# Performance work log

Measured on AMD Instinct MI355X. Metric: run time of the kernel, lower is better.

## Reference

```python
import jax, jax.numpy as jnp
import numpy as np

N, E, B = 100000, 400000, 2048     # nodes, edges, graphs
H, L = 300, 5                      # hidden_feats, n_layers
NT, EF, T = 120, 16, 128           # num_node_types, in_edge_feats, n_tasks
EPS = 1e-5                         # BatchNorm eps (eval mode, running_mean=0, running_var=1)


def setup_inputs() -> dict:
    key = jax.random.key(0)
    ks = jax.random.split(key, 16)
    g = lambda i, shape, s=0.05: jax.random.normal(ks[i], shape, jnp.float32) * s
    return dict(
        node_types=jax.random.randint(ks[0], (N,), 0, NT),
        src=jax.random.randint(ks[1], (E,), 0, N),
        dst=jax.random.randint(ks[2], (E,), 0, N),
        graph_ids=jnp.sort(jax.random.randint(ks[3], (N,), 0, B)),
        edge_feats=jax.random.normal(ks[4], (E, EF), jnp.float32),
        node_emb=g(5, (NT, H), 1.0),          # nn.Embedding(num_node_types, H)
        Wn=g(6, (L, H, H)), bn=g(7, (L, H), 0.01),      # per-layer node projection
        We=g(8, (L, EF, H)), be=g(9, (L, H), 0.01),     # per-layer edge projection
        root=g(10, (L, H)),                   # per-layer root embedding (Embedding(1,H))
        gamma=1.0 + g(11, (L, H), 0.01), beta=g(12, (L, H), 0.01),  # layer BN
        vn_emb=g(13, (H,)),                   # virtual node embedding (Embedding(1,H))
        W1=g(14, (L - 1, H, 2 * H)), b1=jnp.zeros((L - 1, 2 * H), jnp.float32),
        g1=jnp.ones((L - 1, 2 * H), jnp.float32), be1=jnp.zeros((L - 1, 2 * H), jnp.float32),
        W2=g(15, (L - 1, 2 * H, H)), b2=jnp.zeros((L - 1, H), jnp.float32),
        g2=jnp.ones((L - 1, H), jnp.float32), be2=jnp.zeros((L - 1, H), jnp.float32),
        pW=jax.random.normal(jax.random.fold_in(key, 99), (H, T), jnp.float32) * 0.05,
        pb=jnp.zeros((T,), jnp.float32),
    )


def _bn(x, ga, be_):
    # eval-mode BatchNorm1d with running_mean=0, running_var=1
    return x * (ga / jnp.sqrt(1.0 + EPS)) + be_


def reference(node_types, src, dst, graph_ids, edge_feats, node_emb,
              Wn, bn, We, be, root, gamma, beta, vn_emb,
              W1, b1, g1, be1, W2, b2, g2, be2, pW, pb):
    ones_e = jnp.ones((E,), jnp.float32)
    deg = jax.ops.segment_sum(ones_e, dst, num_segments=N) + 1.0   # in_degrees + 1
    norm = deg ** -0.5
    edge_norm = (norm[src] * norm[dst])[:, None]                   # (E, 1)
    inv_deg = (1.0 / deg)[:, None]                                 # (N, 1)

    h = node_emb[node_types]                      # (N, H) node encoder
    vn = jnp.broadcast_to(vn_emb, (B, H))         # (B, H) virtual node feats

    for l in range(L):
        h = h + vn[graph_ids]                     # dgl.broadcast_nodes
        x = h @ Wn[l] + bn[l]                     # (N, H)
        e = edge_feats @ We[l] + be[l]            # (E, H)
        m = edge_norm * jax.nn.relu(x[src] + e)   # per-edge messages
        agg = jax.ops.segment_sum(m, dst, num_segments=N)          # (N, H)
        out = agg + jax.nn.relu(x + root[l]) * inv_deg
        out = _bn(out, gamma[l], beta[l])
        if l != L - 1:
            out = jax.nn.relu(out)
        h_in = h                                  # h_list[l] (after vn broadcast add)
        h = out                                   # dropout p=0 -> identity; residual=False
        if l < L - 1:
            vtmp = jax.ops.segment_sum(h_in, graph_ids, num_segments=B) + vn
            z = jax.nn.relu(_bn(vtmp @ W1[l] + b1[l], g1[l], be1[l]))
            vn = jax.nn.relu(_bn(z @ W2[l] + b2[l], g2[l], be2[l]))

    # mean readout over each graph, then linear head
    counts = jax.ops.segment_sum(jnp.ones((N,), jnp.float32), graph_ids, num_segments=B)
    gsum = jax.ops.segment_sum(h, graph_ids, num_segments=B)
    gmean = gsum / jnp.maximum(counts, 1.0)[:, None]
    return gmean @ pW + pb                        # (B, n_tasks)
```

## Files before the change

kernel.cpp:

```cpp
#include <hip/hip_runtime.h>
#include <hip/hip_bf16.h>
#include <hip/hip_fp16.h>

#define N_ 100000
#define MPAD 100096
#define E_ 400000
#define B_ 2048
#define H_ 300
#define KP_ 320
#define L_ 5
#define EF_ 16
#define T_ 128
#define ANODES 8
#define EMAX 128
#define BNS 0.9999950000374997f

typedef unsigned short ushort_t;
typedef short bf16x8 __attribute__((ext_vector_type(8)));
typedef float f32x4 __attribute__((ext_vector_type(4)));
typedef _Float16 h2f __attribute__((ext_vector_type(2)));

__device__ __forceinline__ ushort_t f2b(float v) {
    unsigned u = __float_as_uint(v);
    unsigned r = (u + 0x7FFFu + ((u >> 16) & 1u)) >> 16;
    return (ushort_t)r;
}

__device__ __forceinline__ float b2f(ushort_t u) {
    return __uint_as_float(((unsigned)u) << 16);
}

__device__ __forceinline__ void gl_lds16(const void* g, void* l) {
    __builtin_amdgcn_global_load_lds(
        (const __attribute__((address_space(1))) void*)g,
        (__attribute__((address_space(3))) void*)l, 16, 0, 0);
}

__device__ __forceinline__ int swzcol(int r, int j) {
    int u = ((j >> 3) & 3) ^ ((r >> 1) & 3);
    return (j & ~31) | (u << 3) | (j & 7);
}

__global__ void k_hist(const int* __restrict__ dst, int* __restrict__ degi, int E) {
    int e = blockIdx.x * blockDim.x + threadIdx.x;
    if (e < E) atomicAdd(&degi[dst[e]], 1);
}

__global__ void k_norm(const int* __restrict__ degi, float* __restrict__ nrm,
                       float* __restrict__ invdeg, int N) {
    int n = blockIdx.x * blockDim.x + threadIdx.x;
    if (n < N) {
        float d = (float)degi[n] + 1.0f;
        nrm[n] = 1.0f / sqrtf(d);
        invdeg[n] = 1.0f / d;
    }
}

__global__ void k_scan1(const int* __restrict__ in, int* __restrict__ out,
                        int* __restrict__ partial, int N) {
    __shared__ int s[1024];
    int i = blockIdx.x * 1024 + threadIdx.x;
    int v = (i < N) ? in[i] : 0;
    s[threadIdx.x] = v;
    __syncthreads();
    for (int off = 1; off < 1024; off <<= 1) {
        int t = (threadIdx.x >= off) ? s[threadIdx.x - off] : 0;
        __syncthreads();
        s[threadIdx.x] += t;
        __syncthreads();
    }
    if (i < N) out[i] = s[threadIdx.x] - v;
    if (threadIdx.x == 1023) partial[blockIdx.x] = s[1023];
}

__global__ void k_scan2(int* __restrict__ partial, int nb, int* __restrict__ totalOut) {
    __shared__ int sh[128];
    int t = threadIdx.x;
    int v = (t < nb) ? partial[t] : 0;
    sh[t] = v;
    __syncthreads();
    for (int off = 1; off < 128; off <<= 1) {
        int u = (t >= off) ? sh[t - off] : 0;
        __syncthreads();
        sh[t] += u;
        __syncthreads();
    }
    if (t < nb) partial[t] = sh[t] - v;
    if (t == 127) *totalOut = sh[127];
}

__global__ void k_scan3(int* __restrict__ out, const int* __restrict__ partial, int N) {
    int i = blockIdx.x * 1024 + threadIdx.x;
    if (i < N) out[i] += partial[blockIdx.x];
}

__global__ void k_scatter(const int* __restrict__ dst, const int* __restrict__ src,
                          const float* __restrict__ ef, const float* __restrict__ nrm,
                          int* __restrict__ cursor, int2* __restrict__ meta,
                          ushort_t* __restrict__ ef16, int E) {
    int e = blockIdx.x * blockDim.x + threadIdx.x;
    if (e >= E) return;
    int d = dst[e], s = src[e];
    int pos = atomicAdd(&cursor[d], 1);
    int2 md;
    md.x = s * KP_;
    md.y = __float_as_int(nrm[s] * nrm[d]);
    meta[pos] = md;
    const float4* ep = (const float4*)&ef[(size_t)e * EF_];
    float4 e0 = ep[0], e1 = ep[1], e2 = ep[2], e3 = ep[3];
    uint4 ua, ub;
    ua.x = __builtin_bit_cast(unsigned, __floats2half2_rn(e0.x, e0.y));
    ua.y = __builtin_bit_cast(unsigned, __floats2half2_rn(e0.z, e0.w));
    ua.z = __builtin_bit_cast(unsigned, __floats2half2_rn(e1.x, e1.y));
    ua.w = __builtin_bit_cast(unsigned, __floats2half2_rn(e1.z, e1.w));
    ub.x = __builtin_bit_cast(unsigned, __floats2half2_rn(e2.x, e2.y));
    ub.y = __builtin_bit_cast(unsigned, __floats2half2_rn(e2.z, e2.w));
    ub.z = __builtin_bit_cast(unsigned, __floats2half2_rn(e3.x, e3.y));
    ub.w = __builtin_bit_cast(unsigned, __floats2half2_rn(e3.z, e3.w));
    uint4* op = (uint4*)&ef16[(size_t)pos * 16];
    op[0] = ua; op[1] = ub;
}

__global__ void k_rowstart(const int* __restrict__ gid, int* __restrict__ rs, int N, int B) {
    int b = blockIdx.x * blockDim.x + threadIdx.x;
    if (b <= B) {
        int lo = 0, hi = N;
        while (lo < hi) { int mid = (lo + hi) >> 1; if (gid[mid] < b) lo = mid + 1; else hi = mid; }
        rs[b] = lo;
    }
}

__global__ void k_hinit(const int* __restrict__ nt, const float* __restrict__ emb,
                        const float* __restrict__ vn_emb,
                        ushort_t* __restrict__ h_bf) {
    int n = blockIdx.x; int j = threadIdx.x;
    if (j >= KP_) return;
    float v = (j < H_) ? emb[(size_t)nt[n] * H_ + j] + vn_emb[j] : 0.f;
    h_bf[(size_t)n * KP_ + swzcol(n, j)] = f2b(v);
}

__global__ void k_vninit(const float* __restrict__ vn_emb, float* __restrict__ vn) {
    int b = blockIdx.x; int j = threadIdx.x;
    if (j >= H_) return;
    vn[(size_t)b * H_ + j] = vn_emb[j];
}

__global__ void k_convW(const float* __restrict__ W, ushort_t* __restrict__ WT,
                        int nl, int K, int Nout, int KPv, int NPBv) {
    int UPR = KPv / 8;
    int tot = nl * NPBv * UPR;
    int idx = blockIdx.x * 256 + threadIdx.x;
    if (idx >= tot) return;
    int l = idx / (NPBv * UPR); int r = idx % (NPBv * UPR);
    int n = r / UPR; int ku = r % UPR;
    int k0 = ku * 8;
    int swz = (ku & 3) ^ ((n >> 1) & 3);
    size_t d = ((size_t)l * NPBv + n) * KPv + (size_t)(k0 & ~31) + swz * 8;
    #pragma unroll
    for (int i = 0; i < 8; i++) {
        int k = k0 + i;
        float v = (k < K && n < Nout) ? W[((size_t)l * K + k) * Nout + n] : 0.f;
        WT[d + i] = f2b(v);
    }
}

__global__ void k_convWeh(const float* __restrict__ We, unsigned* __restrict__ Weh) {
    int idx = blockIdx.x * 256 + threadIdx.x;
    if (idx >= L_ * 8 * H_) return;
    int l = idx / (8 * H_); int r = idx % (8 * H_);
    int k2 = r / H_; int j = r % H_;
    float a = We[((size_t)l * EF_ + 2 * k2) * H_ + j];
    float b = We[((size_t)l * EF_ + 2 * k2 + 1) * H_ + j];
    Weh[((size_t)l * 8 + k2) * H_ + j] = __builtin_bit_cast(unsigned, __floats2half2_rn(a, b));
}

#define MB 128
#define NB 128
__launch_bounds__(256)
__global__ void k_bgemm(const ushort_t* __restrict__ A, const ushort_t* __restrict__ BT,
                        int M, int Nn, int KP,
                        const float* __restrict__ bias, const float* __restrict__ scale,
                        const float* __restrict__ shift, int relu,
                        float* __restrict__ Cf, int ldf,
                        ushort_t* __restrict__ Cb, int ldb, int swzout) {
    __shared__ ushort_t As[MB * 32];
    __shared__ ushort_t Bs[NB * 32];
    int tid = threadIdx.x;
    int lane = tid & 63, wid = tid >> 6;
    int wm = wid >> 1, wn = wid & 1;
    int m0 = blockIdx.x * MB, n0 = blockIdx.y * NB;
    f32x4 acc[4][4];
    #pragma unroll
    for (int mi = 0; mi < 4; mi++)
        #pragma unroll
        for (int ni = 0; ni < 4; ni++)
            acc[mi][ni] = (f32x4){0.f, 0.f, 0.f, 0.f};

    const ushort_t* Ab = A + (size_t)m0 * KP;
    const ushort_t* Bb = BT + (size_t)n0 * KP;
    int lr = lane & 15, lg = lane >> 4;

    for (int k0 = 0; k0 < KP; k0 += 32) {
        #pragma unroll
        for (int i = 0; i < 2; i++) {
            int li = tid + 256 * i;
            int r = li >> 2, u = li & 3;
            gl_lds16(Ab + (size_t)r * KP + k0 + u * 8, &As[(size_t)(li & ~63) * 8]);
        }
        #pragma unroll
        for (int i = 0; i < 2; i++) {
            int li = tid + 256 * i;
            int r = li >> 2, u = li & 3;
            gl_lds16(Bb + (size_t)r * KP + k0 + u * 8, &Bs[(size_t)(li & ~63) * 8]);
        }
        __syncthreads();
        bf16x8 af[4], bv[4];
        #pragma unroll
        for (int mi = 0; mi < 4; mi++) {
            int rr = wm * 64 + mi * 16 + lr;
            int uu = lg ^ ((rr >> 1) & 3);
            af[mi] = *(const bf16x8*)&As[rr * 32 + uu * 8];
        }
        #pragma unroll
        for (int ni = 0; ni < 4; ni++) {
            int rr = wn * 64 + ni * 16 + lr;
            int uu = lg ^ ((rr >> 1) & 3);
            bv[ni] = *(const bf16x8*)&Bs[rr * 32 + uu * 8];
        }
        #pragma unroll
        for (int mi = 0; mi < 4; mi++)
            #pragma unroll
            for (int ni = 0; ni < 4; ni++)
                acc[mi][ni] = __builtin_amdgcn_mfma_f32_16x16x32_bf16(
                    af[mi], bv[ni], acc[mi][ni], 0, 0, 0);
        __syncthreads();
    }

    #pragma unroll
    for (int ni = 0; ni < 4; ni++) {
        int gn = n0 + wn * 64 + ni * 16 + lr;
        if (gn >= Nn) continue;
        float bvv = bias[gn];
        float sc = scale ? scale[gn] * BNS : 0.f;
        float sh = shift ? shift[gn] : 0.f;
        #pragma unroll
        for (int mi = 0; mi < 4; mi++) {
            #pragma unroll
            for (int t = 0; t < 4; t++) {
                int gm = m0 + wm * 64 + mi * 16 + lg * 4 + t;
                if (gm >= M) continue;
                float v = acc[mi][ni][t] + bvv;
                if (scale) v = v * sc + sh;
                if (relu) v = fmaxf(v, 0.f);
                if (Cf) Cf[(size_t)gm * ldf + gn] = v;
                else    Cb[(size_t)gm * ldb + (swzout ? swzcol(gm, gn) : gn)] = f2b(v);
            }
        }
    }
}

__launch_bounds__(256)
__global__ void k_vtmp(const ushort_t* __restrict__ h_bf, const float* __restrict__ vn,
                       const int* __restrict__ rs, ushort_t* __restrict__ vtmp_bf) {
    __shared__ float red[40 * 8 * 6];
    int b = blockIdx.x;
    int t = threadIdx.x;
    int u = t % 40, rr = t / 40;
    int s = rs[b], e = rs[b + 1];
    if (rr < 6) {
        float a8[8] = {0.f, 0.f, 0.f, 0.f, 0.f, 0.f, 0.f, 0.f};
        int g = u >> 2, w = u & 3;
        for (int n = s + rr; n < e; n += 6) {
            int phys = (g << 2) | (w ^ ((n >> 1) & 3));
            bf16x8 hv = *(const bf16x8*)&h_bf[(size_t)n * KP_ + phys * 8];
            #pragma unroll
            for (int k = 0; k < 8; k++) a8[k] += b2f((ushort_t)hv[k]);
        }
        #pragma unroll
        for (int k = 0; k < 8; k++) red[(u * 8 + k) * 6 + rr] = a8[k];
    }
    __syncthreads();
    if (t < 40) {
        int g = t >> 2, w = t & 3;
        int phys = (g << 2) | (w ^ ((b >> 1) & 3));
        ushort_t ov[8];
        #pragma unroll
        for (int k = 0; k < 8; k++) {
            int j = t * 8 + k;
            float sum = 0.f;
            #pragma unroll
            for (int r = 0; r < 6; r++) sum += red[(t * 8 + k) * 6 + r];
            float val = (j < H_) ? sum + vn[(size_t)b * H_ + j] : 0.f;
            ov[k] = f2b(val);
        }
        *(bf16x8*)&vtmp_bf[(size_t)b * KP_ + phys * 8] = *(bf16x8*)ov;
    }
}

__launch_bounds__(256)
__global__ void k_readout(const ushort_t* __restrict__ h_bf, const int* __restrict__ rs,
                          const float* __restrict__ pW, const float* __restrict__ pb,
                          float* __restrict__ out) {
    __shared__ float red[40 * 8 * 6];
    __shared__ float gg[320];
    int b = blockIdx.x;
    int t = threadIdx.x;
    int u = t % 40, rr = t / 40;
    int s = rs[b], e = rs[b + 1];
    if (rr < 6) {
        float a8[8] = {0.f, 0.f, 0.f, 0.f, 0.f, 0.f, 0.f, 0.f};
        int g = u >> 2, w = u & 3;
        for (int n = s + rr; n < e; n += 6) {
            int phys = (g << 2) | (w ^ ((n >> 1) & 3));
            bf16x8 hv = *(const bf16x8*)&h_bf[(size_t)n * KP_ + phys * 8];
            #pragma unroll
            for (int k = 0; k < 8; k++) a8[k] += b2f((ushort_t)hv[k]);
        }
        #pragma unroll
        for (int k = 0; k < 8; k++) red[(u * 8 + k) * 6 + rr] = a8[k];
    }
    __syncthreads();
    if (t < 40) {
        int cnt = e - s; if (cnt < 1) cnt = 1;
        float ic = 1.f / (float)cnt;
        #pragma unroll
        for (int k = 0; k < 8; k++) {
            float sum = 0.f;
            #pragma unroll
            for (int r = 0; r < 6; r++) sum += red[(t * 8 + k) * 6 + r];
            gg[t * 8 + k] = sum * ic;
        }
    }
    __syncthreads();
    if (t < T_) {
        float o = pb[t];
        #pragma unroll 4
        for (int k = 0; k < H_; k++) o = fmaf(gg[k], pW[(size_t)k * T_ + t], o);
        out[(size_t)b * T_ + t] = o;
    }
}

__device__ __forceinline__ float eproj8d(const uint4& ea, const uint4& eb,
                                         const h2f* wh, float bej) {
    float ev = bej;
    ev = __builtin_amdgcn_fdot2(__builtin_bit_cast(h2f, ea.x), wh[0], ev, false);
    ev = __builtin_amdgcn_fdot2(__builtin_bit_cast(h2f, ea.y), wh[1], ev, false);
    ev = __builtin_amdgcn_fdot2(__builtin_bit_cast(h2f, ea.z), wh[2], ev, false);
    ev = __builtin_amdgcn_fdot2(__builtin_bit_cast(h2f, ea.w), wh[3], ev, false);
    ev = __builtin_amdgcn_fdot2(__builtin_bit_cast(h2f, eb.x), wh[4], ev, false);
    ev = __builtin_amdgcn_fdot2(__builtin_bit_cast(h2f, eb.y), wh[5], ev, false);
    ev = __builtin_amdgcn_fdot2(__builtin_bit_cast(h2f, eb.z), wh[6], ev, false);
    ev = __builtin_amdgcn_fdot2(__builtin_bit_cast(h2f, eb.w), wh[7], ev, false);
    return ev;
}

__launch_bounds__(320)
__global__ void k_agg(const ushort_t* __restrict__ x_bf,
                      ushort_t* __restrict__ h_bf,
                      const int* __restrict__ off, const int2* __restrict__ meta,
                      const ushort_t* __restrict__ ef16,
                      const unsigned* __restrict__ Weh_l, const float* __restrict__ be_l,
                      const float* __restrict__ invdeg,
                      const float* __restrict__ root_l, const float* __restrict__ gamma_l,
                      const float* __restrict__ beta_l,
                      const float* __restrict__ vn_next, const int* __restrict__ gid,
                      int relu) {
    __shared__ int2 s_md[EMAX];
    __shared__ unsigned s_ef[EMAX * 8];
    int n0 = blockIdx.x * ANODES;
    int tid = threadIdx.x;
    int j = tid;

    int offv[ANODES + 1];
    #pragma unroll
    for (int k = 0; k <= ANODES; k++) offv[k] = off[n0 + k];
    int estart = offv[0], cnt = offv[ANODES] - estart;
    bool lds_ok = cnt <= EMAX;

    if (lds_ok) {
        const unsigned* efu = (const unsigned*)ef16;
        for (int t = tid; t < cnt; t += 320) s_md[t] = meta[estart + t];
        for (int uu = tid; uu < 8 * cnt; uu += 320)
            s_ef[uu] = efu[(size_t)estart * 8 + uu];
    }
    __syncthreads();

    if (j >= H_) return;
    h2f wh[8];
    #pragma unroll
    for (int k2 = 0; k2 < 8; k2++)
        wh[k2] = __builtin_bit_cast(h2f, Weh_l[k2 * H_ + j]);
    float bej = be_l[j];

    float xn[ANODES];
    #pragma unroll
    for (int ln = 0; ln < ANODES; ln++)
        xn[ln] = b2f(x_bf[(size_t)(n0 + ln) * KP_ + j]);

    float accv[ANODES];
    #pragma unroll
    for (int ln = 0; ln < ANODES; ln++) {
        int rel = offv[ln] - estart, rend = offv[ln + 1] - estart;
        float a = 0.f;
        for (int q = rel; q < rend; q += 4) {
            int i0 = q;
            int i1 = (q + 1 < rend) ? q + 1 : rend - 1;
            int i2 = (q + 2 < rend) ? q + 2 : rend - 1;
            int i3 = (q + 3 < rend) ? q + 3 : rend - 1;
            int2 m0 = lds_ok ? s_md[i0] : meta[estart + i0];
            int2 m1 = lds_ok ? s_md[i1] : meta[estart + i1];
            int2 m2 = lds_ok ? s_md[i2] : meta[estart + i2];
            int2 m3 = lds_ok ? s_md[i3] : meta[estart + i3];
            float en0 = __int_as_float(m0.y);
            float en1 = (q + 1 < rend) ? __int_as_float(m1.y) : 0.f;
            float en2 = (q + 2 < rend) ? __int_as_float(m2.y) : 0.f;
            float en3 = (q + 3 < rend) ? __int_as_float(m3.y) : 0.f;
            float xv0 = b2f(x_bf[(size_t)m0.x + j]);
            float xv1 = b2f(x_bf[(size_t)m1.x + j]);
            float xv2 = b2f(x_bf[(size_t)m2.x + j]);
            float xv3 = b2f(x_bf[(size_t)m3.x + j]);
            uint4 a0, b0, a1, b1, a2, b2, a3, b3;
            if (lds_ok) {
                a0 = *(const uint4*)&s_ef[i0 * 8]; b0 = *(const uint4*)&s_ef[i0 * 8 + 4];
                a1 = *(const uint4*)&s_ef[i1 * 8]; b1 = *(const uint4*)&s_ef[i1 * 8 + 4];
                a2 = *(const uint4*)&s_ef[i2 * 8]; b2 = *(const uint4*)&s_ef[i2 * 8 + 4];
                a3 = *(const uint4*)&s_ef[i3 * 8]; b3 = *(const uint4*)&s_ef[i3 * 8 + 4];
            } else {
                const uint4* p0 = (const uint4*)&ef16[(size_t)(estart + i0) * 16];
                const uint4* p1 = (const uint4*)&ef16[(size_t)(estart + i1) * 16];
                const uint4* p2 = (const uint4*)&ef16[(size_t)(estart + i2) * 16];
                const uint4* p3 = (const uint4*)&ef16[(size_t)(estart + i3) * 16];
                a0 = p0[0]; b0 = p0[1]; a1 = p1[0]; b1 = p1[1];
                a2 = p2[0]; b2 = p2[1]; a3 = p3[0]; b3 = p3[1];
            }
            a = fmaf(en0, fmaxf(xv0 + eproj8d(a0, b0, wh, bej), 0.f), a);
            a = fmaf(en1, fmaxf(xv1 + eproj8d(a1, b1, wh, bej), 0.f), a);
            a = fmaf(en2, fmaxf(xv2 + eproj8d(a2, b2, wh, bej), 0.f), a);
            a = fmaf(en3, fmaxf(xv3 + eproj8d(a3, b3, wh, bej), 0.f), a);
        }
        accv[ln] = a;
    }

    float rootj = root_l[j], gmj = gamma_l[j] * BNS, btj = beta_l[j];
    #pragma unroll
    for (int ln = 0; ln < ANODES; ln++) {
        int n = n0 + ln;
        float v = accv[ln] + fmaxf(xn[ln] + rootj, 0.f) * invdeg[n];
        v = v * gmj + btj;
        if (relu) v = fmaxf(v, 0.f);
        if (vn_next) v += vn_next[(size_t)gid[n] * H_ + j];
        h_bf[(size_t)n * KP_ + swzcol(n, j)] = f2b(v);
    }
}

extern "C" void kernel_launch(void* const* d_in, const int* in_sizes, int n_in,
                              void* d_out, int out_size, void* d_ws, size_t ws_size,
                              hipStream_t stream) {
    const int* node_types = (const int*)d_in[0];
    const int* src        = (const int*)d_in[1];
    const int* dst        = (const int*)d_in[2];
    const int* graph_ids  = (const int*)d_in[3];
    const float* edge_feats = (const float*)d_in[4];
    const float* node_emb   = (const float*)d_in[5];
    const float* Wn   = (const float*)d_in[6];
    const float* bn   = (const float*)d_in[7];
    const float* We   = (const float*)d_in[8];
    const float* be   = (const float*)d_in[9];
    const float* root = (const float*)d_in[10];
    const float* gamma = (const float*)d_in[11];
    const float* beta  = (const float*)d_in[12];
    const float* vn_emb = (const float*)d_in[13];
    const float* W1  = (const float*)d_in[14];
    const float* b1  = (const float*)d_in[15];
    const float* g1  = (const float*)d_in[16];
    const float* be1 = (const float*)d_in[17];
    const float* W2  = (const float*)d_in[18];
    const float* b2  = (const float*)d_in[19];
    const float* g2  = (const float*)d_in[20];
    const float* be2 = (const float*)d_in[21];
    const float* pW  = (const float*)d_in[22];
    const float* pb  = (const float*)d_in[23];
    float* out = (float*)d_out;

    char* p = (char*)d_ws;
    auto alloc = [&](size_t bytes) { void* q = (void*)p; p += (bytes + 255) & ~(size_t)255; return q; };
    ushort_t* h_bf   = (ushort_t*)alloc((size_t)MPAD * KP_ * 2);
    ushort_t* x_bf   = (ushort_t*)alloc((size_t)MPAD * KP_ * 2);
    ushort_t* ef16   = (ushort_t*)alloc((size_t)E_ * 16 * 2);
    ushort_t* WnT    = (ushort_t*)alloc((size_t)L_ * 384 * KP_ * 2);
    unsigned* Weh    = (unsigned*)alloc((size_t)L_ * 8 * H_ * 4);
    ushort_t* W1T    = (ushort_t*)alloc((size_t)4 * 640 * KP_ * 2);
    ushort_t* W2T    = (ushort_t*)alloc((size_t)4 * 384 * 640 * 2);
    ushort_t* vtmp_bf= (ushort_t*)alloc((size_t)B_ * KP_ * 2);
    ushort_t* z_bf   = (ushort_t*)alloc((size_t)B_ * 640 * 2);
    float* vn    = (float*)alloc((size_t)B_ * H_ * 4);
    float* nrm   = (float*)alloc((size_t)N_ * 4);
    float* invdeg= (float*)alloc((size_t)N_ * 4);
    int* degi    = (int*)alloc((size_t)N_ * 4);
    int* csr_off = (int*)alloc((size_t)(N_ + 1) * 4);
    int* cursor  = (int*)alloc((size_t)N_ * 4);
    int2* meta   = (int2*)alloc((size_t)E_ * 8);
    int* rs      = (int*)alloc((size_t)(B_ + 1) * 4);
    int* partial = (int*)alloc((size_t)128 * 4);

    const int SCAN_NB = (N_ + 1023) / 1024;

    hipMemsetAsync(degi, 0, (size_t)N_ * 4, stream);
    k_hist<<<(E_ + 255) / 256, 256, 0, stream>>>(dst, degi, E_);
    k_norm<<<(N_ + 255) / 256, 256, 0, stream>>>(degi, nrm, invdeg, N_);

    k_scan1<<<SCAN_NB, 1024, 0, stream>>>(degi, csr_off, partial, N_);
    k_scan2<<<1, 128, 0, stream>>>(partial, SCAN_NB, csr_off + N_);
    k_scan3<<<SCAN_NB, 1024, 0, stream>>>(csr_off, partial, N_);
    hipMemcpyAsync(cursor, csr_off, (size_t)N_ * 4, hipMemcpyDeviceToDevice, stream);
    k_scatter<<<(E_ + 255) / 256, 256, 0, stream>>>(dst, src, edge_feats, nrm,
                                                    cursor, meta, ef16, E_);

    k_rowstart<<<(B_ + 1 + 255) / 256, 256, 0, stream>>>(graph_ids, rs, N_, B_);

    k_convW<<<(L_ * 384 * (KP_ / 8) + 255) / 256, 256, 0, stream>>>(Wn, WnT, L_, H_, H_, KP_, 384);
    k_convWeh<<<(L_ * 8 * H_ + 255) / 256, 256, 0, stream>>>(We, Weh);
    k_convW<<<(4 * 640 * (KP_ / 8) + 255) / 256, 256, 0, stream>>>(W1, W1T, 4, H_, 2 * H_, KP_, 640);
    k_convW<<<(4 * 384 * (640 / 8) + 255) / 256, 256, 0, stream>>>(W2, W2T, 4, 2 * H_, H_, 640, 384);

    k_hinit<<<N_, 320, 0, stream>>>(node_types, node_emb, vn_emb, h_bf);
    k_vninit<<<B_, 320, 0, stream>>>(vn_emb, vn);

    dim3 gx(MPAD / MB, 3);
    dim3 gz(B_ / MB, 5);
    dim3 gv(B_ / MB, 3);

    for (int l = 0; l < L_; l++) {
        k_bgemm<<<gx, 256, 0, stream>>>(h_bf, WnT + (size_t)l * 384 * KP_,
                                        N_, H_, KP_,
                                        bn + (size_t)l * H_, nullptr, nullptr, 0,
                                        nullptr, 0, x_bf, KP_, 0);
        if (l < L_ - 1) {
            k_vtmp<<<B_, 256, 0, stream>>>(h_bf, vn, rs, vtmp_bf);
            k_bgemm<<<gz, 256, 0, stream>>>(vtmp_bf, W1T + (size_t)l * 640 * KP_,
                                            B_, 2 * H_, KP_,
                                            b1 + (size_t)l * 2 * H_,
                                            g1 + (size_t)l * 2 * H_, be1 + (size_t)l * 2 * H_, 1,
                                            nullptr, 0, z_bf, 640, 1);
            k_bgemm<<<gv, 256, 0, stream>>>(z_bf, W2T + (size_t)l * 384 * 640,
                                            B_, H_, 640,
                                            b2 + (size_t)l * H_,
                                            g2 + (size_t)l * H_, be2 + (size_t)l * H_, 1,
                                            vn, H_, nullptr, 0, 0);
        }
        k_agg<<<N_ / ANODES, 320, 0, stream>>>(x_bf, h_bf, csr_off, meta, ef16,
                                               Weh + (size_t)l * 8 * H_, be + (size_t)l * H_,
                                               invdeg,
                                               root + (size_t)l * H_,
                                               gamma + (size_t)l * H_, beta + (size_t)l * H_,
                                               (l < L_ - 1) ? vn : nullptr, graph_ids,
                                               (l < L_ - 1) ? 1 : 0);
    }

    k_readout<<<B_, 256, 0, stream>>>(h_bf, rs, pW, pb, out);
}
```

Before: 1.772 ms.

## Compute per-edge projections with MFMA into LDS inside aggregation kernel

Edge features are now stored as zero-padded bf16 rows of 32, and the edge weight matrix is pre-transposed to bf16. Inside k_agg, each block computes the edge-feature projection for all of its edges with 16x16x32 bf16 MFMA into a shared tile, replacing the per-thread fp16 dot2 chains that each of the 300 threads ran for every edge. Nodes per block drop from 8 to 4 and the edge cap from 128 to 64 so the projection tile fits in LDS. This adds bf16 rounding of the projection, doubles the edge-feature storage and the block count, and uses a scalar fp32 fallback path for blocks that exceed the edge cap.

```diff
diff --git a/kernel.cpp b/kernel.cpp
--- a/kernel.cpp
+++ b/kernel.cpp
@@ -11,14 +11,15 @@
 #define L_ 5
 #define EF_ 16
 #define T_ 128
-#define ANODES 8
-#define EMAX 128
+#define ANODES 4
+#define EMAX 64
+#define EPAD 66
+#define NT19 19
 #define BNS 0.9999950000374997f
 
 typedef unsigned short ushort_t;
 typedef short bf16x8 __attribute__((ext_vector_type(8)));
 typedef float f32x4 __attribute__((ext_vector_type(4)));
-typedef _Float16 h2f __attribute__((ext_vector_type(2)));
 
 __device__ __forceinline__ ushort_t f2b(float v) {
     unsigned u = __float_as_uint(v);
@@ -97,7 +98,7 @@
 __global__ void k_scatter(const int* __restrict__ dst, const int* __restrict__ src,
                           const float* __restrict__ ef, const float* __restrict__ nrm,
                           int* __restrict__ cursor, int2* __restrict__ meta,
-                          ushort_t* __restrict__ ef16, int E) {
+                          ushort_t* __restrict__ ef_bf, int E) {
     int e = blockIdx.x * blockDim.x + threadIdx.x;
     if (e >= E) return;
     int d = dst[e], s = src[e];
@@ -106,19 +107,15 @@
     md.x = s * KP_;
     md.y = __float_as_int(nrm[s] * nrm[d]);
     meta[pos] = md;
-    const float4* ep = (const float4*)&ef[(size_t)e * EF_];
-    float4 e0 = ep[0], e1 = ep[1], e2 = ep[2], e3 = ep[3];
-    uint4 ua, ub;
-    ua.x = __builtin_bit_cast(unsigned, __floats2half2_rn(e0.x, e0.y));
-    ua.y = __builtin_bit_cast(unsigned, __floats2half2_rn(e0.z, e0.w));
-    ua.z = __builtin_bit_cast(unsigned, __floats2half2_rn(e1.x, e1.y));
-    ua.w = __builtin_bit_cast(unsigned, __floats2half2_rn(e1.z, e1.w));
-    ub.x = __builtin_bit_cast(unsigned, __floats2half2_rn(e2.x, e2.y));
-    ub.y = __builtin_bit_cast(unsigned, __floats2half2_rn(e2.z, e2.w));
-    ub.z = __builtin_bit_cast(unsigned, __floats2half2_rn(e3.x, e3.y));
-    ub.w = __builtin_bit_cast(unsigned, __floats2half2_rn(e3.z, e3.w));
-    uint4* op = (uint4*)&ef16[(size_t)pos * 16];
-    op[0] = ua; op[1] = ub;
+    const float* epf = &ef[(size_t)e * EF_];
+    ushort_t row[16];
+    #pragma unroll
+    for (int k = 0; k < EF_; k++) row[k] = f2b(epf[k]);
+    uint4* op = (uint4*)&ef_bf[(size_t)pos * 32];
+    op[0] = *(uint4*)&row[0];
+    op[1] = *(uint4*)&row[8];
+    op[2] = (uint4){0u, 0u, 0u, 0u};
+    op[3] = (uint4){0u, 0u, 0u, 0u};
 }
 
 __global__ void k_rowstart(const int* __restrict__ gid, int* __restrict__ rs, int N, int B) {
@@ -164,14 +161,21 @@
     }
 }
 
-__global__ void k_convWeh(const float* __restrict__ We, unsigned* __restrict__ Weh) {
+__global__ void k_convWe32(const float* __restrict__ We, ushort_t* __restrict__ WeT32) {
     int idx = blockIdx.x * 256 + threadIdx.x;
-    if (idx >= L_ * 8 * H_) return;
-    int l = idx / (8 * H_); int r = idx % (8 * H_);
-    int k2 = r / H_; int j = r % H_;
-    float a = We[((size_t)l * EF_ + 2 * k2) * H_ + j];
-    float b = We[((size_t)l * EF_ + 2 * k2 + 1) * H_ + j];
-    Weh[((size_t)l * 8 + k2) * H_ + j] = __builtin_bit_cast(unsigned, __floats2half2_rn(a, b));
+    if (idx >= L_ * 320) return;
+    int l = idx / 320; int n = idx % 320;
+    ushort_t row[32];
+    #pragma unroll
+    for (int k = 0; k < 32; k++) {
+        float v = (k < EF_ && n < H_) ? We[((size_t)l * EF_ + k) * H_ + n] : 0.f;
+        row[k] = f2b(v);
+    }
+    uint4* dst = (uint4*)&WeT32[(size_t)idx * 32];
+    dst[0] = *(uint4*)&row[0];
+    dst[1] = *(uint4*)&row[8];
+    dst[2] = *(uint4*)&row[16];
+    dst[3] = *(uint4*)&row[24];
 }
 
 #define MB 128
@@ -340,56 +344,54 @@
     }
 }
 
-__device__ __forceinline__ float eproj8d(const uint4& ea, const uint4& eb,
-                                         const h2f* wh, float bej) {
-    float ev = bej;
-    ev = __builtin_amdgcn_fdot2(__builtin_bit_cast(h2f, ea.x), wh[0], ev, false);
-    ev = __builtin_amdgcn_fdot2(__builtin_bit_cast(h2f, ea.y), wh[1], ev, false);
-    ev = __builtin_amdgcn_fdot2(__builtin_bit_cast(h2f, ea.z), wh[2], ev, false);
-    ev = __builtin_amdgcn_fdot2(__builtin_bit_cast(h2f, ea.w), wh[3], ev, false);
-    ev = __builtin_amdgcn_fdot2(__builtin_bit_cast(h2f, eb.x), wh[4], ev, false);
-    ev = __builtin_amdgcn_fdot2(__builtin_bit_cast(h2f, eb.y), wh[5], ev, false);
-    ev = __builtin_amdgcn_fdot2(__builtin_bit_cast(h2f, eb.z), wh[6], ev, false);
-    ev = __builtin_amdgcn_fdot2(__builtin_bit_cast(h2f, eb.w), wh[7], ev, false);
-    return ev;
-}
-
 __launch_bounds__(320)
 __global__ void k_agg(const ushort_t* __restrict__ x_bf,
                       ushort_t* __restrict__ h_bf,
                       const int* __restrict__ off, const int2* __restrict__ meta,
-                      const ushort_t* __restrict__ ef16,
-                      const unsigned* __restrict__ Weh_l, const float* __restrict__ be_l,
+                      const ushort_t* __restrict__ ef_bf,
+                      const ushort_t* __restrict__ WeT32_l,
+                      const float* __restrict__ Wef_l,
+                      const float* __restrict__ be_l,
                       const float* __restrict__ invdeg,
                       const float* __restrict__ root_l, const float* __restrict__ gamma_l,
                       const float* __restrict__ beta_l,
                       const float* __restrict__ vn_next, const int* __restrict__ gid,
                       int relu) {
+    __shared__ ushort_t s_ep[320 * EPAD];
     __shared__ int2 s_md[EMAX];
-    __shared__ unsigned s_ef[EMAX * 8];
     int n0 = blockIdx.x * ANODES;
     int tid = threadIdx.x;
-    int j = tid;
+    int lane = tid & 63, wv = tid >> 6;
+    int lr = lane & 15, lg = lane >> 4;
 
     int offv[ANODES + 1];
     #pragma unroll
     for (int k = 0; k <= ANODES; k++) offv[k] = off[n0 + k];
     int estart = offv[0], cnt = offv[ANODES] - estart;
-    bool lds_ok = cnt <= EMAX;
-
-    if (lds_ok) {
-        const unsigned* efu = (const unsigned*)ef16;
+    bool fast = cnt <= EMAX;
+
+    if (fast) {
         for (int t = tid; t < cnt; t += 320) s_md[t] = meta[estart + t];
-        for (int uu = tid; uu < 8 * cnt; uu += 320)
-            s_ef[uu] = efu[(size_t)estart * 8 + uu];
+        int mt = (cnt + 15) >> 4;
+        for (int mi = 0; mi < mt; mi++) {
+            bf16x8 av = *(const bf16x8*)&ef_bf[(size_t)(estart + mi * 16 + lr) * 32 + lg * 8];
+            for (int ni = wv; ni < NT19; ni += 5) {
+                bf16x8 bv = *(const bf16x8*)&WeT32_l[(size_t)(ni * 16 + lr) * 32 + lg * 8];
+                f32x4 c = (f32x4){0.f, 0.f, 0.f, 0.f};
+                c = __builtin_amdgcn_mfma_f32_16x16x32_bf16(av, bv, c, 0, 0, 0);
+                unsigned lo = (unsigned)f2b(c[0]) | ((unsigned)f2b(c[1]) << 16);
+                unsigned hi = (unsigned)f2b(c[2]) | ((unsigned)f2b(c[3]) << 16);
+                int col = ni * 16 + lr;
+                int row = mi * 16 + lg * 4;
+                *(unsigned*)&s_ep[col * EPAD + row] = lo;
+                *(unsigned*)&s_ep[col * EPAD + row + 2] = hi;
+            }
+        }
     }
     __syncthreads();
 
+    int j = tid;
     if (j >= H_) return;
-    h2f wh[8];
-    #pragma unroll
-    for (int k2 = 0; k2 < 8; k2++)
-        wh[k2] = __builtin_bit_cast(h2f, Weh_l[k2 * H_ + j]);
     float bej = be_l[j];
 
     float xn[ANODES];
@@ -398,47 +400,54 @@
         xn[ln] = b2f(x_bf[(size_t)(n0 + ln) * KP_ + j]);
 
     float accv[ANODES];
-    #pragma unroll
-    for (int ln = 0; ln < ANODES; ln++) {
-        int rel = offv[ln] - estart, rend = offv[ln + 1] - estart;
-        float a = 0.f;
-        for (int q = rel; q < rend; q += 4) {
-            int i0 = q;
-            int i1 = (q + 1 < rend) ? q + 1 : rend - 1;
-            int i2 = (q + 2 < rend) ? q + 2 : rend - 1;
-            int i3 = (q + 3 < rend) ? q + 3 : rend - 1;
-            int2 m0 = lds_ok ? s_md[i0] : meta[estart + i0];
-            int2 m1 = lds_ok ? s_md[i1] : meta[estart + i1];
-            int2 m2 = lds_ok ? s_md[i2] : meta[estart + i2];
-            int2 m3 = lds_ok ? s_md[i3] : meta[estart + i3];
-            float en0 = __int_as_float(m0.y);
-            float en1 = (q + 1 < rend) ? __int_as_float(m1.y) : 0.f;
-            float en2 = (q + 2 < rend) ? __int_as_float(m2.y) : 0.f;
-            float en3 = (q + 3 < rend) ? __int_as_float(m3.y) : 0.f;
-            float xv0 = b2f(x_bf[(size_t)m0.x + j]);
-            float xv1 = b2f(x_bf[(size_t)m1.x + j]);
-            float xv2 = b2f(x_bf[(size_t)m2.x + j]);
-            float xv3 = b2f(x_bf[(size_t)m3.x + j]);
-            uint4 a0, b0, a1, b1, a2, b2, a3, b3;
-            if (lds_ok) {
-                a0 = *(const uint4*)&s_ef[i0 * 8]; b0 = *(const uint4*)&s_ef[i0 * 8 + 4];
-                a1 = *(const uint4*)&s_ef[i1 * 8]; b1 = *(const uint4*)&s_ef[i1 * 8 + 4];
-                a2 = *(const uint4*)&s_ef[i2 * 8]; b2 = *(const uint4*)&s_ef[i2 * 8 + 4];
-                a3 = *(const uint4*)&s_ef[i3 * 8]; b3 = *(const uint4*)&s_ef[i3 * 8 + 4];
-            } else {
-                const uint4* p0 = (const uint4*)&ef16[(size_t)(estart + i0) * 16];
-                const uint4* p1 = (const uint4*)&ef16[(size_t)(estart + i1) * 16];
-                const uint4* p2 = (const uint4*)&ef16[(size_t)(estart + i2) * 16];
-                const uint4* p3 = (const uint4*)&ef16[(size_t)(estart + i3) * 16];
-                a0 = p0[0]; b0 = p0[1]; a1 = p1[0]; b1 = p1[1];
-                a2 = p2[0]; b2 = p2[1]; a3 = p3[0]; b3 = p3[1];
+    if (fast) {
+        int jb = j * EPAD;
+        #pragma unroll
+        for (int ln = 0; ln < ANODES; ln++) {
+            int rel = offv[ln] - estart, rend = offv[ln + 1] - estart;
+            float a = 0.f;
+            for (int q = rel; q < rend; q += 4) {
+                int i0 = q;
+                int i1 = (q + 1 < rend) ? q + 1 : rend - 1;
+                int i2 = (q + 2 < rend) ? q + 2 : rend - 1;
+                int i3 = (q + 3 < rend) ? q + 3 : rend - 1;
+                int2 m0 = s_md[i0], m1 = s_md[i1], m2 = s_md[i2], m3 = s_md[i3];
+                float en0 = __int_as_float(m0.y);
+                float en1 = (q + 1 < rend) ? __int_as_float(m1.y) : 0.f;
+                float en2 = (q + 2 < rend) ? __int_as_float(m2.y) : 0.f;
+                float en3 = (q + 3 < rend) ? __int_as_float(m3.y) : 0.f;
+                float xv0 = b2f(x_bf[(size_t)m0.x + j]);
+                float xv1 = b2f(x_bf[(size_t)m1.x + j]);
+                float xv2 = b2f(x_bf[(size_t)m2.x + j]);
+                float xv3 = b2f(x_bf[(size_t)m3.x + j]);
+                float e0 = b2f(s_ep[jb + i0]);
+                float e1 = b2f(s_ep[jb + i1]);
+                float e2 = b2f(s_ep[jb + i2]);
+                float e3 = b2f(s_ep[jb + i3]);
+                a = fmaf(en0, fmaxf(xv0 + e0 + bej, 0.f), a);
+                a = fmaf(en1, fmaxf(xv1 + e1 + bej, 0.f), a);
+                a = fmaf(en2, fmaxf(xv2 + e2 + bej, 0.f), a);
+                a = fmaf(en3, fmaxf(xv3 + e3 + bej, 0.f), a);
             }
-            a = fmaf(en0, fmaxf(xv0 + eproj8d(a0, b0, wh, bej), 0.f), a);
-            a = fmaf(en1, fmaxf(xv1 + eproj8d(a1, b1, wh, bej), 0.f), a);
-            a = fmaf(en2, fmaxf(xv2 + eproj8d(a2, b2, wh, bej), 0.f), a);
-            a = fmaf(en3, fmaxf(xv3 + eproj8d(a3, b3, wh, bej), 0.f), a);
-        }
-        accv[ln] = a;
+            accv[ln] = a;
+        }
+    } else {
+        #pragma unroll
+        for (int ln = 0; ln < ANODES; ln++) {
+            int rel = offv[ln] - estart, rend = offv[ln + 1] - estart;
+            float a = 0.f;
+            for (int q = rel; q < rend; q++) {
+                int2 m = meta[estart + q];
+                float xv = b2f(x_bf[(size_t)m.x + j]);
+                float ev = bej;
+                const ushort_t* er = &ef_bf[(size_t)(estart + q) * 32];
+                #pragma unroll
+                for (int k = 0; k < EF_; k++)
+                    ev = fmaf(b2f(er[k]), Wef_l[k * H_ + j], ev);
+                a = fmaf(__int_as_float(m.y), fmaxf(xv + ev, 0.f), a);
+            }
+            accv[ln] = a;
+        }
     }
 
     float rootj = root_l[j], gmj = gamma_l[j] * BNS, btj = beta_l[j];
@@ -486,9 +495,9 @@
     auto alloc = [&](size_t bytes) { void* q = (void*)p; p += (bytes + 255) & ~(size_t)255; return q; };
     ushort_t* h_bf   = (ushort_t*)alloc((size_t)MPAD * KP_ * 2);
     ushort_t* x_bf   = (ushort_t*)alloc((size_t)MPAD * KP_ * 2);
-    ushort_t* ef16   = (ushort_t*)alloc((size_t)E_ * 16 * 2);
+    ushort_t* ef_bf  = (ushort_t*)alloc((size_t)(E_ + 64) * 32 * 2);
     ushort_t* WnT    = (ushort_t*)alloc((size_t)L_ * 384 * KP_ * 2);
-    unsigned* Weh    = (unsigned*)alloc((size_t)L_ * 8 * H_ * 4);
+    ushort_t* WeT32  = (ushort_t*)alloc((size_t)L_ * 320 * 32 * 2);
     ushort_t* W1T    = (ushort_t*)alloc((size_t)4 * 640 * KP_ * 2);
     ushort_t* W2T    = (ushort_t*)alloc((size_t)4 * 384 * 640 * 2);
     ushort_t* vtmp_bf= (ushort_t*)alloc((size_t)B_ * KP_ * 2);
@@ -514,12 +523,12 @@
     k_scan3<<<SCAN_NB, 1024, 0, stream>>>(csr_off, partial, N_);
     hipMemcpyAsync(cursor, csr_off, (size_t)N_ * 4, hipMemcpyDeviceToDevice, stream);
     k_scatter<<<(E_ + 255) / 256, 256, 0, stream>>>(dst, src, edge_feats, nrm,
-                                                    cursor, meta, ef16, E_);
+                                                    cursor, meta, ef_bf, E_);
 
     k_rowstart<<<(B_ + 1 + 255) / 256, 256, 0, stream>>>(graph_ids, rs, N_, B_);
 
     k_convW<<<(L_ * 384 * (KP_ / 8) + 255) / 256, 256, 0, stream>>>(Wn, WnT, L_, H_, H_, KP_, 384);
-    k_convWeh<<<(L_ * 8 * H_ + 255) / 256, 256, 0, stream>>>(We, Weh);
+    k_convWe32<<<(L_ * 320 + 255) / 256, 256, 0, stream>>>(We, WeT32);
     k_convW<<<(4 * 640 * (KP_ / 8) + 255) / 256, 256, 0, stream>>>(W1, W1T, 4, H_, 2 * H_, KP_, 640);
     k_convW<<<(4 * 384 * (640 / 8) + 255) / 256, 256, 0, stream>>>(W2, W2T, 4, 2 * H_, H_, 640, 384);
 
@@ -548,8 +557,10 @@
                                             g2 + (size_t)l * H_, be2 + (size_t)l * H_, 1,
                                             vn, H_, nullptr, 0, 0);
         }
-        k_agg<<<N_ / ANODES, 320, 0, stream>>>(x_bf, h_bf, csr_off, meta, ef16,
-                                               Weh + (size_t)l * 8 * H_, be + (size_t)l * H_,
+        k_agg<<<N_ / ANODES, 320, 0, stream>>>(x_bf, h_bf, csr_off, meta, ef_bf,
+                                               WeT32 + (size_t)l * 320 * 32,
+                                               We + (size_t)l * EF_ * H_,
+                                               be + (size_t)l * H_,
                                                invdeg,
                                                root + (size_t)l * H_,
                                                gamma + (size_t)l * H_, beta + (size_t)l * H_,
```

Result: slower. 2.448 ms (+38.2%).
